# Kernel optimization log

Measured on AMD Instinct MI355X. Metric: run time of the kernel, lower is better.

Reference implementation:

```python
import jax, jax.numpy as jnp
import numpy as np


def _lenet(x, cw1, cb1, cw2, cb2, fw1, fb1, fw2, fb2, fw3, fb3):
    # x: [B,1,28,28] -> [B,10] softmax probs (Conv -> MaxPool -> ReLU, twice)
    y = jax.lax.conv_general_dilated(x, cw1, (1, 1), 'VALID') + cb1[None, :, None, None]
    y = jax.lax.reduce_window(y, -jnp.inf, jax.lax.max, (1, 1, 2, 2), (1, 1, 2, 2), 'VALID')
    y = jax.nn.relu(y)
    y = jax.lax.conv_general_dilated(y, cw2, (1, 1), 'VALID') + cb2[None, :, None, None]
    y = jax.lax.reduce_window(y, -jnp.inf, jax.lax.max, (1, 1, 2, 2), (1, 1, 2, 2), 'VALID')
    y = jax.nn.relu(y)
    y = y.reshape(y.shape[0], -1)  # [B, 16*4*4]
    y = jax.nn.relu(y @ fw1.T + fb1)
    y = jax.nn.relu(y @ fw2.T + fb2)
    return jax.nn.softmax(y @ fw3.T + fb3, axis=1)


def setup_inputs() -> dict:
    key = jax.random.key(0)
    ks = jax.random.split(key, 11)
    B = 16384
    inp = {
        'x': jax.random.normal(ks[0], (B, 2, 28, 28), dtype=jnp.float32),
        'cw1': jax.random.normal(ks[1], (6, 1, 5, 5), dtype=jnp.float32) * 0.2,
        'cb1': jax.random.normal(ks[2], (6,), dtype=jnp.float32) * 0.1,
        'cw2': jax.random.normal(ks[3], (16, 6, 5, 5), dtype=jnp.float32) * 0.08,
        'cb2': jax.random.normal(ks[4], (16,), dtype=jnp.float32) * 0.1,
        'fw1': jax.random.normal(ks[5], (120, 256), dtype=jnp.float32) * 0.0625,
        'fb1': jax.random.normal(ks[6], (120,), dtype=jnp.float32) * 0.05,
        'fw2': jax.random.normal(ks[7], (84, 120), dtype=jnp.float32) * 0.09,
        'fb2': jax.random.normal(ks[8], (84,), dtype=jnp.float32) * 0.05,
        'fw3': jax.random.normal(ks[9], (10, 84), dtype=jnp.float32) * 0.1,
        'fb3': jax.random.normal(ks[10], (10,), dtype=jnp.float32) * 0.05,
    }
    return inp


def reference(x, cw1, cb1, cw2, cb2, fw1, fb1, fw2, fb2, fw3, fb3):
    p1 = _lenet(x[:, 0:1], cw1, cb1, cw2, cb2, fw1, fb1, fw2, fb2, fw3, fb3)  # [B,10]
    p2 = _lenet(x[:, 1:2], cw1, cb1, cw2, cb2, fw1, fb1, fw2, fb2, fw3, fb3)  # [B,10]
    # torch Conv1d with weight=flip(p2[i]) and padding=K-1 is the full linear
    # convolution z[t] = sum_j p2[j] * p1[t-j], length 2*10-1 = 19.
    # p2 is treated as a constant (copied under no_grad in the original).
    p2c = jax.lax.stop_gradient(p2)
    Z = jax.vmap(lambda a, b: jnp.convolve(a, b, mode='full'))(p1, p2c)  # [B,19]
    return jnp.log(Z)
```

## Files before the change

kernel.cpp:

```cpp
#include <hip/hip_runtime.h>
#include <math.h>


#define SPB 8
#define P1H_IN 440
#define P1H_IC 144

typedef _Float16 f16x2 __attribute__((ext_vector_type(2)));
typedef _Float16 half4 __attribute__((ext_vector_type(4)));
typedef _Float16 half8 __attribute__((ext_vector_type(8)));
typedef float floatx4 __attribute__((ext_vector_type(4)));
typedef float floatx16 __attribute__((ext_vector_type(16)));

#define WS_F2  8192
#define WS_C1B 11264
#define WS_C2A 11456
#define WS_C2K 11776
#define WS_TOT 12096

__global__ __launch_bounds__(256) void prep_ws(
    const float* __restrict__ fw1, const float* __restrict__ fw2,
    const float* __restrict__ cw1, const float* __restrict__ cw2,
    uint4* __restrict__ ws)
{
    int idx = blockIdx.x * 256 + threadIdx.x;
    if (idx >= WS_TOT) return;
    if (idx < WS_F2) {
        int l = idx & 63, ks = (idx >> 6) & 15, ot = idx >> 10;
        int cn = l & 15, g = l >> 4;
        int o = ot * 16 + cn, k0 = ks * 16 + g * 4;
        union { uint4 u; _Float16 h[8]; } r;
        for (int j = 0; j < 4; ++j) {
            float w = (o < 120) ? fw1[o * 256 + k0 + j] : 0.f;
            r.h[2 * j] = (_Float16)w; r.h[2 * j + 1] = r.h[2 * j];
        }
        ws[idx] = r.u;
    } else if (idx < WS_C1B) {
        int e = idx - WS_F2;
        int l = e & 63, ks = (e >> 6) & 7, ot = e >> 9;
        int cn = l & 15, g = l >> 4;
        int o = ot * 16 + cn, k0 = ks * 16 + g * 4;
        union { uint4 u; _Float16 h[8]; } r;
        for (int j = 0; j < 4; ++j) {
            float w = (o < 84 && k0 + j < 120) ? fw2[o * 120 + k0 + j] : 0.f;
            r.h[2 * j] = (_Float16)w; r.h[2 * j + 1] = r.h[2 * j];
        }
        ws[idx] = r.u;
    } else if (idx < WS_C2A) {
        int e = idx - WS_C1B; int l = e & 63; int ks = e >> 6;
        int l5 = l >> 5, cn = l & 31, s = cn >> 3, ch = cn & 7;
        int ky = 2 * ks + l5;
        union { uint4 u; _Float16 h[8]; } r;
        for (int j = 0; j < 8; ++j) {
            int kx = j - s;
            float w = (ch < 6 && ky < 5 && kx >= 0 && kx <= 4)
                    ? cw1[ch * 25 + ky * 5 + kx] : 0.f;
            r.h[j] = (_Float16)w;
        }
        ws[idx] = r.u;
    } else if (idx < WS_C2K) {
        int e = idx - WS_C2A; int l = e & 63; int ks = e >> 6;
        int cn = l & 15, g = l >> 4;
        union { uint4 u; _Float16 h[8]; } r;
        for (int j = 0; j < 8; ++j) {
            int hidx = ks * 32 + g * 8 + j;
            int kp = hidx >> 1, el = hidx & 1;
            float w = 0.f;
            if (kp < 75) {
                int icp = kp / 25, rr = kp % 25;
                w = cw2[cn * 150 + (2 * icp + el) * 25 + rr];
            }
            r.h[j] = (_Float16)w;
        }
        ws[idx] = r.u;
    } else {
        int e = idx - WS_C2K; int l = e & 63; int ks = e >> 6;
        int g = l >> 4;
        union { uint4 u; int i[4]; } r;
        for (int j = 0; j < 4; ++j) {
            int kp = ks * 16 + g * 4 + j;
            kp = kp > 74 ? 74 : kp;
            int icp = kp / 25, rr = kp % 25, ky = rr / 5, kx = rr % 5;
            r.i[j] = icp * P1H_IC + ky * 12 + kx;
        }
        ws[idx] = r.u;
    }
}

__global__ __launch_bounds__(256, 4) void lenet_fused(
    const float* __restrict__ x,
    const float* __restrict__ cb1,
    const float* __restrict__ cb2,
    const float* __restrict__ fb1,
    const float* __restrict__ fb2,
    const float* __restrict__ fw3,
    const float* __restrict__ fb3,
    const uint4* __restrict__ ws4,
    float* __restrict__ out)
{
    const int tid = threadIdx.x;
    const int b0  = blockIdx.x * SPB;

    __shared__ __align__(16) float s_pool[3072];
    __shared__ __align__(16) f16x2 s_p1h [16 * P1H_IN];

    uint32_t* s_u32 = (uint32_t*)s_pool;
    uint32_t* p1u   = (uint32_t*)s_p1h;
    float* s_log = s_pool + 2912;

    const int lane = tid & 63;
    const int wv   = tid >> 6;

    {
        const int l5   = lane >> 5;
        const int cn   = lane & 31;
        const int s    = cn >> 3;
        const int ch   = cn & 7;
        const int Y0   = cn < 24 ? cn : 23;

        half8 bfr[3];
#pragma unroll
        for (int ks = 0; ks < 3; ++ks) {
            union { uint4 u; half8 h; } t;
            t.u = ws4[WS_C1B + ks * 64 + lane];
            bfr[ks] = t.h;
        }
        const float bch = (ch < 6) ? cb1[ch] : 0.f;
        const bool  wrl = ((s & 1) == 0) && (ch < 6);
        _Float16* p1w = (_Float16*)s_p1h;
        _Float16* ipbase = (_Float16*)(s_u32 + wv * 392);
        const float4* xbase = (const float4*)(x + (size_t)b0 * 1568);

        floatx16 zero16 = {0.f,0.f,0.f,0.f, 0.f,0.f,0.f,0.f,
                           0.f,0.f,0.f,0.f, 0.f,0.f,0.f,0.f};

        float4 qreg[4];
#pragma unroll
        for (int j = 0; j < 4; ++j) {
            int i = j * 64 + lane;
            if (i < 196) qreg[j] = xbase[wv * 196 + i];
        }

#pragma unroll 1
        for (int p = 0; p < 4; ++p) {
            const int inst = wv + 4 * p;
            {
                ushort4* sh = (ushort4*)ipbase;
#pragma unroll
                for (int j = 0; j < 4; ++j) {
                    int i = j * 64 + lane;
                    if (i < 196) {
                        float4 q = qreg[j];
                        union { ushort4 u; _Float16 h[4]; } w;
                        w.h[0] = (_Float16)q.x; w.h[1] = (_Float16)q.y;
                        w.h[2] = (_Float16)q.z; w.h[3] = (_Float16)q.w;
                        sh[i] = w.u;
                    }
                }
            }
            if (p < 3) {
#pragma unroll
                for (int j = 0; j < 4; ++j) {
                    int i = j * 64 + lane;
                    if (i < 196) qreg[j] = xbase[(inst + 4) * 196 + i];
                }
            }
            asm volatile("s_waitcnt lgkmcnt(0)" ::: "memory");

            const int wb = (inst * P1H_IN + (ch >> 1) * P1H_IC) * 2 + (ch & 1);

#pragma unroll 1
            for (int c = 0; c < 3; ++c) {
                floatx16 acc0 = zero16, acc1 = zero16;
#pragma unroll
                for (int ks = 0; ks < 3; ++ks) {
                    int ra = Y0 + 2 * ks + l5;
                    ra = ra > 27 ? 27 : ra;
                    const _Float16* rp = ipbase + ra * 28 + c * 8;
                    union { half8 h8; half4 h4[2]; } a0, a1;
                    a0.h4[0] = *(const half4*)(rp);
                    a0.h4[1] = *(const half4*)(rp + 4);
                    a1.h4[0] = a0.h4[1];
                    a1.h4[1] = *(const half4*)(rp + 8);
                    acc0 = __builtin_amdgcn_mfma_f32_32x32x16_f16(
                        a0.h8, bfr[ks], acc0, 0, 0, 0);
                    acc1 = __builtin_amdgcn_mfma_f32_32x32x16_f16(
                        a1.h8, bfr[ks], acc1, 0, 0, 0);
                }
#pragma unroll
                for (int h = 0; h < 2; ++h) {
                    const int xbi = 2 * c + h;
                    const int px2 = (xbi * 2 + (s >> 1)) * 2;
#pragma unroll
                    for (int d = 0; d < 4; ++d) {
#pragma unroll
                        for (int cp = 0; cp < 2; ++cp) {
                            float e0 = h ? acc1[4 * d + 2 * cp]
                                         : acc0[4 * d + 2 * cp];
                            float e1 = h ? acc1[4 * d + 2 * cp + 1]
                                         : acc0[4 * d + 2 * cp + 1];
                            float vy = fmaxf(e0, e1);
                            float vo = __shfl_xor(vy, 8);
                            float vp = fmaxf(vy, vo);
                            float r  = fmaxf(vp + bch, 0.f);
                            int  py  = cp + 4 * d + 2 * l5;
                            if (wrl && py < 12)
                                p1w[wb + py * 24 + px2] = (_Float16)r;
                        }
                    }
                }
            }
        }
    }
    asm volatile("s_waitcnt lgkmcnt(0)" ::: "memory");

    {
        const int g  = lane >> 4;
        const int cn = lane & 15;

        half8 afr[5];
        int4  kot[5];
#pragma unroll
        for (int ks = 0; ks < 5; ++ks) {
            union { uint4 u; half8 h; } t;
            t.u = ws4[WS_C2A + ks * 64 + lane];
            afr[ks] = t.h;
            union { uint4 u; int4 i; } k;
            k.u = ws4[WS_C2K + ks * 64 + lane];
            kot[ks] = k.i;
        }

        float bias4[4];
#pragma unroll
        for (int r = 0; r < 4; ++r) bias4[r] = cb2[g * 4 + r];

        const int csb = (cn >> 3) * 12 + (cn & 7);
        const int px = (lane & 7) >> 1;
        const bool wrp = (lane & 9) == 0;

        floatx4 zero4 = {0.f, 0.f, 0.f, 0.f};

#pragma unroll 1
        for (int ih = 0; ih < 4; ++ih) {
            const int inst = wv + 4 * ih;
            const f16x2* pb = s_p1h + inst * P1H_IN + csb;

            floatx4 acc[4] = {zero4, zero4, zero4, zero4};
#pragma unroll
            for (int ks = 0; ks < 5; ++ks) {
                const int k0 = kot[ks].x, k1 = kot[ks].y,
                          k2 = kot[ks].z, k3 = kot[ks].w;
#pragma unroll
                for (int ntl = 0; ntl < 4; ++ntl) {
                    union { half8 h8; f16x2 h2[4]; } bp;
                    bp.h2[0] = pb[k0 + 24 * ntl];
                    bp.h2[1] = pb[k1 + 24 * ntl];
                    bp.h2[2] = pb[k2 + 24 * ntl];
                    bp.h2[3] = pb[k3 + 24 * ntl];
                    acc[ntl] = __builtin_amdgcn_mfma_f32_16x16x32_f16(
                        afr[ks], bp.h8, acc[ntl], 0, 0, 0);
                }
            }

            uint32_t* p2o = p1u + inst * 440 + px;
#pragma unroll
            for (int ntl = 0; ntl < 4; ++ntl) {
#pragma unroll
                for (int r = 0; r < 4; ++r) {
                    float v = acc[ntl][r];
                    v = fmaxf(v, __shfl_xor(v, 1));
                    v = fmaxf(v, __shfl_xor(v, 8));
                    v = fmaxf(v + bias4[r], 0.f);
                    _Float16 hi = (_Float16)v;
                    _Float16 lo = (_Float16)(v - (float)hi);
                    f16x2 pr; pr.x = hi; pr.y = lo;
                    if (wrp) p2o[(g * 4 + r) * 16 + ntl * 4] =
                        __builtin_bit_cast(uint32_t, pr);
                }
            }
        }
    }
    __syncthreads();

    {
        const int cn = lane & 15, g4 = lane >> 4;
        const uint4* apb4 = (const uint4*)(p1u + cn * 440);
        const uint4* bw0 = ws4 + (size_t)wv * 1024 + lane;
        const uint4* bw1 = ws4 + (size_t)(wv + 4) * 1024 + lane;
        floatx4 acc0 = {0.f,0.f,0.f,0.f}, acc1 = {0.f,0.f,0.f,0.f};
#pragma unroll 4
        for (int ks = 0; ks < 16; ++ks) {
            union { half8 h; uint4 u; } af;
            af.u = apb4[ks * 4 + g4];
            union { half8 h; uint4 u; } b0, b1;
            b0.u = bw0[ks * 64]; b1.u = bw1[ks * 64];
            acc0 = __builtin_amdgcn_mfma_f32_16x16x32_f16(af.h, b0.h, acc0, 0,0,0);
            acc1 = __builtin_amdgcn_mfma_f32_16x16x32_f16(af.h, b1.h, acc1, 0,0,0);
        }
#pragma unroll
        for (int t = 0; t < 2; ++t) {
            int o = (wv + 4 * t) * 16 + cn;
            floatx4 a = t ? acc1 : acc0;
            float bias = (o < 120) ? fb1[o] : 0.f;
#pragma unroll
            for (int r = 0; r < 4; ++r) {
                int inst = g4 * 4 + r;
                float v = fmaxf(a[r] + bias, 0.f);
                if (o >= 120) v = 0.f;
                _Float16 hi = (_Float16)v;
                _Float16 lo = (_Float16)(v - (float)hi);
                f16x2 pr; pr.x = hi; pr.y = lo;
                p1u[inst * 440 + 264 + o] = __builtin_bit_cast(uint32_t, pr);
            }
        }
    }
    __syncthreads();

    {
        const int cn = lane & 15, g4 = lane >> 4;
        const uint4* apb4 = (const uint4*)(p1u + cn * 440 + 264);
        const uint4* bw0 = ws4 + WS_F2 + (size_t)wv * 512 + lane;
        const uint4* bw1 = bw0 + 2048;
        const bool has1 = wv < 2;
        floatx4 acc0 = {0.f,0.f,0.f,0.f}, acc1 = {0.f,0.f,0.f,0.f};
#pragma unroll 4
        for (int ks = 0; ks < 8; ++ks) {
            union { half8 h; uint4 u; } af;
            af.u = apb4[ks * 4 + g4];
            union { half8 h; uint4 u; } b0;
            b0.u = bw0[ks * 64];
            acc0 = __builtin_amdgcn_mfma_f32_16x16x32_f16(af.h, b0.h, acc0, 0,0,0);
            if (has1) {
                union { half8 h; uint4 u; } b1;
                b1.u = bw1[ks * 64];
                acc1 = __builtin_amdgcn_mfma_f32_16x16x32_f16(af.h, b1.h, acc1, 0,0,0);
            }
        }
        float* s_f2 = (float*)(s_u32 + 1568);
#pragma unroll
        for (int t = 0; t < 2; ++t) {
            if (t && !has1) break;
            int o = (wv + 4 * t) * 16 + cn;
            floatx4 a = t ? acc1 : acc0;
            if (o < 84) {
                float bias = fb2[o];
#pragma unroll
                for (int r = 0; r < 4; ++r) {
                    int inst = g4 * 4 + r;
                    s_f2[inst * 84 + o] = fmaxf(a[r] + bias, 0.f);
                }
            }
        }
    }
    __syncthreads();

    if (tid < 160) {
        int o    = tid % 10;
        int inst = tid / 10;
        const float4* wr = (const float4*)(fw3 + o * 84);
        const float4* q0 = (const float4*)(s_pool + 1568 + inst * 84);
        float a0 = 0.f;
#pragma unroll
        for (int k = 0; k < 21; ++k) {
            float4 w4 = wr[k];
            float4 p = q0[k];
            a0 = fmaf(w4.x,p.x,a0); a0 = fmaf(w4.y,p.y,a0); a0 = fmaf(w4.z,p.z,a0); a0 = fmaf(w4.w,p.w,a0);
        }
        s_log[inst * 10 + o] = a0 + fb3[o];
    }
    __syncthreads();

    if (tid < 19 * SPB) {
        int ls = tid / 19;
        int t  = tid % 19;
        const float* la = &s_log[(ls * 2 + 0) * 10];
        const float* lb = &s_log[(ls * 2 + 1) * 10];
        float pa[10], pb[10];
        float mxa = la[0], mxb = lb[0];
#pragma unroll
        for (int j = 1; j < 10; ++j) { mxa = fmaxf(mxa, la[j]); mxb = fmaxf(mxb, lb[j]); }
        float sa = 0.f, sb = 0.f;
#pragma unroll
        for (int j = 0; j < 10; ++j) {
            pa[j] = __expf(la[j] - mxa); sa += pa[j];
            pb[j] = __expf(lb[j] - mxb); sb += pb[j];
        }
        float inv = 1.f / (sa * sb);
        int jlo = t - 9 > 0 ? t - 9 : 0;
        int jhi = t < 9 ? t : 9;
        float z = 0.f;
        for (int j = jlo; j <= jhi; ++j)
            z += pa[j] * pb[t - j];
        out[(size_t)(b0 + ls) * 19 + t] = __logf(z * inv);
    }
}

extern "C" void kernel_launch(void* const* d_in, const int* in_sizes, int n_in,
                              void* d_out, int out_size, void* d_ws, size_t ws_size,
                              hipStream_t stream) {
    const float* x   = (const float*)d_in[0];
    const float* cw1 = (const float*)d_in[1];
    const float* cb1 = (const float*)d_in[2];
    const float* cw2 = (const float*)d_in[3];
    const float* cb2 = (const float*)d_in[4];
    const float* fw1 = (const float*)d_in[5];
    const float* fb1 = (const float*)d_in[6];
    const float* fw2 = (const float*)d_in[7];
    const float* fb2 = (const float*)d_in[8];
    const float* fw3 = (const float*)d_in[9];
    const float* fb3 = (const float*)d_in[10];
    float* out = (float*)d_out;
    uint4* ws4 = (uint4*)d_ws;

    const int B = in_sizes[0] / (2 * 28 * 28);

    prep_ws<<<(WS_TOT + 255) / 256, 256, 0, stream>>>(fw1, fw2, cw1, cw2, ws4);
    lenet_fused<<<B / SPB, 256, 0, stream>>>(x, cb1, cb2,
                                             fb1, fb2, fw3, fb3, ws4, out);
}
```

Baseline: 224.4 us.

## Micro-optimize conv1 pooling epilogue, conv2 operand loads, and fc1 unroll

Makes the first three input-staging loop iterations unconditional with clamped indexing for the last one. Pools the conv1 output in packed fp16 pairs so one shuffle covers two rows instead of one per row. Batches the conv2 B-operand LDS loads ahead of the MFMA chain and raises the fc1 unroll from 4 to 8. These aim to cut shuffle count and branch overhead and to improve load scheduling. The cost is more registers, and the max/ReLU now runs in fp16 after bias rounding.

```diff
diff --git a/kernel.cpp b/kernel.cpp
--- a/kernel.cpp
+++ b/kernel.cpp
@@ -138,7 +138,7 @@
 #pragma unroll
         for (int j = 0; j < 4; ++j) {
             int i = j * 64 + lane;
-            if (i < 196) qreg[j] = xbase[wv * 196 + i];
+            if (j < 3 || i < 196) qreg[j] = xbase[wv * 196 + (j < 3 ? i : (i < 196 ? i : 0))];
         }
 
 #pragma unroll 1
@@ -149,12 +149,12 @@
 #pragma unroll
                 for (int j = 0; j < 4; ++j) {
                     int i = j * 64 + lane;
-                    if (i < 196) {
+                    if (j < 3 || i < 196) {
                         float4 q = qreg[j];
                         union { ushort4 u; _Float16 h[4]; } w;
                         w.h[0] = (_Float16)q.x; w.h[1] = (_Float16)q.y;
                         w.h[2] = (_Float16)q.z; w.h[3] = (_Float16)q.w;
-                        sh[i] = w.u;
+                        sh[j < 3 ? i : (i < 196 ? i : 0)] = w.u;
                     }
                 }
             }
@@ -162,7 +162,8 @@
 #pragma unroll
                 for (int j = 0; j < 4; ++j) {
                     int i = j * 64 + lane;
-                    if (i < 196) qreg[j] = xbase[(inst + 4) * 196 + i];
+                    if (j < 3 || i < 196)
+                        qreg[j] = xbase[(inst + 4) * 196 + (j < 3 ? i : (i < 196 ? i : 0))];
                 }
             }
             asm volatile("s_waitcnt lgkmcnt(0)" ::: "memory");
@@ -193,19 +194,27 @@
                     const int px2 = (xbi * 2 + (s >> 1)) * 2;
 #pragma unroll
                     for (int d = 0; d < 4; ++d) {
-#pragma unroll
-                        for (int cp = 0; cp < 2; ++cp) {
-                            float e0 = h ? acc1[4 * d + 2 * cp]
-                                         : acc0[4 * d + 2 * cp];
-                            float e1 = h ? acc1[4 * d + 2 * cp + 1]
-                                         : acc0[4 * d + 2 * cp + 1];
-                            float vy = fmaxf(e0, e1);
-                            float vo = __shfl_xor(vy, 8);
-                            float vp = fmaxf(vy, vo);
-                            float r  = fmaxf(vp + bch, 0.f);
-                            int  py  = cp + 4 * d + 2 * l5;
-                            if (wrl && py < 12)
-                                p1w[wb + py * 24 + px2] = (_Float16)r;
+                        float e00 = h ? acc1[4 * d + 0] : acc0[4 * d + 0];
+                        float e01 = h ? acc1[4 * d + 1] : acc0[4 * d + 1];
+                        float e10 = h ? acc1[4 * d + 2] : acc0[4 * d + 2];
+                        float e11 = h ? acc1[4 * d + 3] : acc0[4 * d + 3];
+                        float vb0 = fmaxf(e00, e01) + bch;
+                        float vb1 = fmaxf(e10, e11) + bch;
+                        f16x2 pk; pk.x = (_Float16)vb0; pk.y = (_Float16)vb1;
+                        int po_i = __shfl_xor(__builtin_bit_cast(int, pk), 8);
+                        f16x2 po = __builtin_bit_cast(f16x2, po_i);
+                        f16x2 pm;
+                        pm.x = pk.x > po.x ? pk.x : po.x;
+                        pm.y = pk.y > po.y ? pk.y : po.y;
+                        _Float16 z = (_Float16)0.f;
+                        pm.x = pm.x > z ? pm.x : z;
+                        pm.y = pm.y > z ? pm.y : z;
+                        int py0 = 4 * d + 2 * l5;
+                        if (wrl) {
+                            if (py0 < 12)
+                                p1w[wb + py0 * 24 + px2] = pm.x;
+                            if (py0 + 1 < 12)
+                                p1w[wb + (py0 + 1) * 24 + px2] = pm.y;
                         }
                     }
                 }
@@ -248,15 +257,20 @@
             floatx4 acc[4] = {zero4, zero4, zero4, zero4};
 #pragma unroll
             for (int ks = 0; ks < 5; ++ks) {
-                const int k0 = kot[ks].x, k1 = kot[ks].y,
-                          k2 = kot[ks].z, k3 = kot[ks].w;
+                f16x2 bv[4][4];
+#pragma unroll
+                for (int j = 0; j < 4; ++j) {
+                    const int kj = (j == 0) ? kot[ks].x : (j == 1) ? kot[ks].y
+                                 : (j == 2) ? kot[ks].z : kot[ks].w;
+                    const f16x2* q = pb + kj;
+                    bv[j][0] = q[0];  bv[j][1] = q[24];
+                    bv[j][2] = q[48]; bv[j][3] = q[72];
+                }
 #pragma unroll
                 for (int ntl = 0; ntl < 4; ++ntl) {
                     union { half8 h8; f16x2 h2[4]; } bp;
-                    bp.h2[0] = pb[k0 + 24 * ntl];
-                    bp.h2[1] = pb[k1 + 24 * ntl];
-                    bp.h2[2] = pb[k2 + 24 * ntl];
-                    bp.h2[3] = pb[k3 + 24 * ntl];
+                    bp.h2[0] = bv[0][ntl]; bp.h2[1] = bv[1][ntl];
+                    bp.h2[2] = bv[2][ntl]; bp.h2[3] = bv[3][ntl];
                     acc[ntl] = __builtin_amdgcn_mfma_f32_16x16x32_f16(
                         afr[ks], bp.h8, acc[ntl], 0, 0, 0);
                 }
@@ -288,7 +302,7 @@
         const uint4* bw0 = ws4 + (size_t)wv * 1024 + lane;
         const uint4* bw1 = ws4 + (size_t)(wv + 4) * 1024 + lane;
         floatx4 acc0 = {0.f,0.f,0.f,0.f}, acc1 = {0.f,0.f,0.f,0.f};
-#pragma unroll 4
+#pragma unroll 8
         for (int ks = 0; ks < 16; ++ks) {
             union { half8 h; uint4 u; } af;
             af.u = apb4[ks * 4 + g4];
```

New measurement: 220.1 us. About the same (-1.9%).
